# Performance work log

Measured on AMD Instinct MI355X. Metric: run time of the kernel, lower is better.

The kernel has to match this reference:

```python
import jax, jax.numpy as jnp
import numpy as np

TOP_K = 2
NORM_TOPK_PROB = True


def setup_inputs() -> dict:
    key = jax.random.key(0)
    k1, k2 = jax.random.split(key)
    hidden_states = jax.random.normal(k1, (4, 4096, 2048), dtype=jnp.float32)
    # gate weight [n_routed_experts, hidden_size], kaiming-uniform-like scale
    weight = jax.random.normal(k2, (64, 2048), dtype=jnp.float32) * 0.02
    return {"hidden_states": hidden_states, "weight": weight}


def reference(hidden_states, weight):
    bsz, seq_len, h = hidden_states.shape
    x = hidden_states.reshape(-1, h)                      # [T, H]
    logits = jnp.einsum("th,eh->te", x, weight)           # [T, E]
    scores = jax.nn.softmax(logits, axis=-1)              # [T, E]
    topk_weight, topk_idx = jax.lax.top_k(scores, TOP_K)  # [T, K] each
    if TOP_K > 1 and NORM_TOPK_PROB:
        topk_weight = topk_weight / (topk_weight.sum(axis=-1, keepdims=True) + 1e-20)
    return (topk_idx.reshape(bsz, seq_len, -1), topk_weight.reshape(bsz, seq_len, -1))
```

## Files before the change

kernel.cpp:

```cpp
#include <hip/hip_runtime.h>
#include <math.h>

#define H    2048
#define NE   64
#define TOKB 64
#define KC   32
#define NCH  64
#define NBUF 4
#define TAU  4.0e-3f
#define NEGF (-3.0e38f)

typedef __bf16 bf16x8 __attribute__((ext_vector_type(8)));
typedef float  f32x16 __attribute__((ext_vector_type(16)));

#define MFMA(a, b, c) __builtin_amdgcn_mfma_f32_32x32x16_bf16((a), (b), (c), 0, 0, 0)
#define LD4(p) (*reinterpret_cast<const float4*>(p))

__device__ __forceinline__ void cvt8(const float4 a, const float4 b,
                                     bf16x8& hi, bf16x8& lo) {
    const float v0 = a.x, v1 = a.y, v2 = a.z, v3 = a.w;
    const float v4 = b.x, v5 = b.y, v6 = b.z, v7 = b.w;
    hi[0] = (__bf16)v0; lo[0] = (__bf16)(v0 - (float)hi[0]);
    hi[1] = (__bf16)v1; lo[1] = (__bf16)(v1 - (float)hi[1]);
    hi[2] = (__bf16)v2; lo[2] = (__bf16)(v2 - (float)hi[2]);
    hi[3] = (__bf16)v3; lo[3] = (__bf16)(v3 - (float)hi[3]);
    hi[4] = (__bf16)v4; lo[4] = (__bf16)(v4 - (float)hi[4]);
    hi[5] = (__bf16)v5; lo[5] = (__bf16)(v5 - (float)hi[5]);
    hi[6] = (__bf16)v6; lo[6] = (__bf16)(v6 - (float)hi[6]);
    hi[7] = (__bf16)v7; lo[7] = (__bf16)(v7 - (float)hi[7]);
}

__device__ __forceinline__ void gll16(const void* g, void* l) {
    __builtin_amdgcn_global_load_lds(
        (const __attribute__((address_space(1))) void*)g,
        (__attribute__((address_space(3))) void*)l, 16, 0, 0);
}

__global__ __launch_bounds__(256) void prep_w(
    const float* __restrict__ w, __bf16* __restrict__ wp, int* __restrict__ wl)
{
    const int e   = blockIdx.x;
    const int tid = threadIdx.x;
    if (e == 0 && tid == 0) wl[0] = 0;
    const float4 a = LD4(&w[e * H + tid * 8]);
    const float4 b = LD4(&w[e * H + tid * 8 + 4]);
    bf16x8 hi, lo;
    cvt8(a, b, hi, lo);
    const int c  = tid >> 2;
    const int kk = (tid & 3) * 8;
    *reinterpret_cast<bf16x8*>(wp + e * 4096 + c * 64 + kk)      = hi;
    *reinterpret_cast<bf16x8*>(wp + e * 4096 + c * 64 + 32 + kk) = lo;
}

__global__ __launch_bounds__(256) void moe_gate_mfma(
    const float* __restrict__ x,
    const __bf16* __restrict__ wp,
    float* __restrict__ out, int woff,
    int* __restrict__ wl, int wlcap)
{
    __shared__ float4 lds4[NBUF][1024];

    const int tid  = threadIdx.x;
    const int lane = tid & 63;
    const int wv   = tid >> 6;
    const int mt   = wv >> 1;
    const int kh   = wv & 1;
    const int lo5  = lane & 31;
    const int hi5  = lane >> 5;
    const int t0   = blockIdx.x * TOKB;

    const char* sbase[4];
    #pragma unroll
    for (int s = 0; s < 4; ++s) {
        const int byte = (s * 256 + tid) * 16;
        if (byte < 8192) {
            const int row = byte >> 7;
            const int sl  = ((byte >> 4) & 7) ^ (row & 7);
            sbase[s] = (const char*)wp + (size_t)row * 8192 + sl * 16;
        } else {
            const int b   = byte - 8192;
            const int row = b >> 7;
            const int sl  = ((b >> 4) & 7) ^ (row & 7);
            sbase[s] = (const char*)x + (size_t)(t0 + row) * 8192 + sl * 16;
        }
    }

    f32x16 acc0, acc1;
    #pragma unroll
    for (int i = 0; i < 16; ++i) { acc0[i] = 0.f; acc1[i] = 0.f; }

    #pragma unroll
    for (int p = 0; p < 3; ++p)
        #pragma unroll
        for (int s = 0; s < 4; ++s)
            gll16(sbase[s] + p * 128, &lds4[p][s * 256 + wv * 64]);

    const int ra0 = lo5, ra1 = 32 + lo5;
    const int sA  = kh * 2 + hi5;
    const int offAh0 = ra0 * 128 + (((sA)     ^ (ra0 & 7)) << 4);
    const int offAl0 = ra0 * 128 + (((4 + sA) ^ (ra0 & 7)) << 4);
    const int offAh1 = ra1 * 128 + (((sA)     ^ (ra1 & 7)) << 4);
    const int offAl1 = ra1 * 128 + (((4 + sA) ^ (ra1 & 7)) << 4);
    const int rb  = mt * 32 + lo5;
    const int sB  = kh * 4 + hi5 * 2;
    const int offB0 = 8192 + rb * 128 + (((sB)     ^ (rb & 7)) << 4);
    const int offB1 = 8192 + rb * 128 + (((sB + 1) ^ (rb & 7)) << 4);

    for (int c = 0; c < NCH; ++c) {
        if (c < NCH - 2) {
            asm volatile("s_waitcnt vmcnt(8)" ::: "memory");
        } else if (c == NCH - 2) {
            asm volatile("s_waitcnt vmcnt(4)" ::: "memory");
        } else {
            asm volatile("s_waitcnt vmcnt(0)" ::: "memory");
        }
        __builtin_amdgcn_s_barrier();

        const char* bufb = (const char*)&lds4[c & 3][0];
        const bf16x8 ah0 = *reinterpret_cast<const bf16x8*>(bufb + offAh0);
        const bf16x8 al0 = *reinterpret_cast<const bf16x8*>(bufb + offAl0);
        const bf16x8 ah1 = *reinterpret_cast<const bf16x8*>(bufb + offAh1);
        const bf16x8 al1 = *reinterpret_cast<const bf16x8*>(bufb + offAl1);
        const float4 b1  = *reinterpret_cast<const float4*>(bufb + offB0);
        const float4 b2  = *reinterpret_cast<const float4*>(bufb + offB1);

        bf16x8 bh, bl;
        cvt8(b1, b2, bh, bl);

        acc0 = MFMA(ah0, bh, acc0);
        acc1 = MFMA(ah1, bh, acc1);
        acc0 = MFMA(ah0, bl, acc0);
        acc1 = MFMA(ah1, bl, acc1);
        acc0 = MFMA(al0, bh, acc0);
        acc1 = MFMA(al1, bh, acc1);

        if (c + 3 < NCH) {
            #pragma unroll
            for (int s = 0; s < 4; ++s)
                gll16(sbase[s] + (c + 3) * 128,
                      &lds4[(c + 3) & 3][s * 256 + wv * 64]);
        }
    }

    __syncthreads();
    float* S = reinterpret_cast<float*>(&lds4[0][0]);
    if (kh == 1) {
        const int base = (mt * 32 + lo5) * 65;
        #pragma unroll
        for (int r = 0; r < 16; ++r) {
            const int e0 = (r & 3) + 8 * (r >> 2) + 4 * hi5;
            S[base + e0]      = acc0[r];
            S[base + 32 + e0] = acc1[r];
        }
    }
    __syncthreads();
    if (kh == 1) return;
    {
        const int base = (mt * 32 + lo5) * 65;
        #pragma unroll
        for (int r = 0; r < 16; ++r) {
            const int e0 = (r & 3) + 8 * (r >> 2) + 4 * hi5;
            acc0[r] += S[base + e0];
            acc1[r] += S[base + 32 + e0];
        }
    }

    float m1 = NEGF, m2 = NEGF, m3 = NEGF;
    int   i1 = 0, i2 = 0;
    #pragma unroll
    for (int r = 0; r < 16; ++r) {
        const float v = acc0[r];
        const int   e = (r & 3) + 8 * (r >> 2) + 4 * hi5;
        if (v > m1)      { m3 = m2; m2 = m1; i2 = i1; m1 = v; i1 = e; }
        else if (v > m2) { m3 = m2; m2 = v; i2 = e; }
        else if (v > m3) { m3 = v; }
    }
    #pragma unroll
    for (int r = 0; r < 16; ++r) {
        const float v = acc1[r];
        const int   e = 32 + (r & 3) + 8 * (r >> 2) + 4 * hi5;
        if (v > m1)      { m3 = m2; m2 = m1; i2 = i1; m1 = v; i1 = e; }
        else if (v > m2) { m3 = m2; m2 = v; i2 = e; }
        else if (v > m3) { m3 = v; }
    }

    const float n1 = __shfl_xor(m1, 32), n2 = __shfl_xor(m2, 32), n3 = __shfl_xor(m3, 32);
    const int   j1 = __shfl_xor(i1, 32), j2 = __shfl_xor(i2, 32);

    float a1, a2, a3, b1, b2, b3; int ia1, ia2, ib1, ib2;
    const bool aF = (m1 > n1) || (m1 == n1 && i1 < j1);
    if (aF) { a1=m1; a2=m2; a3=m3; ia1=i1; ia2=i2; b1=n1; b2=n2; b3=n3; ib1=j1; ib2=j2; }
    else    { a1=n1; a2=n2; a3=n3; ia1=j1; ia2=j2; b1=m1; b2=m2; b3=m3; ib1=i1; ib2=i2; }

    const float o1 = a1; const int oi1 = ia1;
    float o2, o3; int oi2;
    const bool a2F = (a2 > b1) || (a2 == b1 && ia2 < ib1);
    if (a2F) { o2 = a2; oi2 = ia2; o3 = (a3 > b1) ? a3 : b1; }
    else     { o2 = b1; oi2 = ib1; o3 = (a2 > b2) ? a2 : b2; }

    if (hi5 == 0) {
        const int t = t0 + mt * 32 + lo5;
        const float r = expf(o2 - o1);
        const float s = 1.0f + r;
        out[2 * t + 0]        = (float)oi1;
        out[2 * t + 1]        = (float)oi2;
        out[woff + 2 * t + 0] = 1.0f / s;
        out[woff + 2 * t + 1] = r / s;
        if ((o1 - o2 < TAU) || (o2 - o3 < TAU)) {
            const int pos = atomicAdd(wl, 1);
            if (pos < wlcap) wl[1 + pos] = t;
        }
    }
}

__global__ __launch_bounds__(256) void moe_refine_fp64(
    const float* __restrict__ x, const float* __restrict__ w,
    float* __restrict__ out, int woff,
    const int* __restrict__ wl, int wlcap)
{
    __shared__ double Sd[3][NE];
    const int lane = threadIdx.x & 63;
    const int wv   = threadIdx.x >> 6;
    const int ks   = wv * 512;
    int cnt = wl[0];
    if (cnt > wlcap) cnt = wlcap;

    for (int i = blockIdx.x; i < cnt; i += gridDim.x) {
        const int t = wl[1 + i];

        const float4 xa = LD4(&x[(size_t)t * H + ks + lane * 4]);
        const float4 xb = LD4(&x[(size_t)t * H + ks + 256 + lane * 4]);
        const double x0 = xa.x, x1 = xa.y, x2 = xa.z, x3 = xa.w;
        const double x4 = xb.x, x5 = xb.y, x6 = xb.z, x7 = xb.w;

        double myacc = 0.0;
        #pragma unroll 4
        for (int e = 0; e < NE; ++e) {
            const float4 wa = LD4(&w[(size_t)e * H + ks + lane * 4]);
            const float4 wb = LD4(&w[(size_t)e * H + ks + 256 + lane * 4]);
            double sA = 0.0, sB = 0.0;
            sA = fma((double)wa.x, x0, sA); sA = fma((double)wa.y, x1, sA);
            sA = fma((double)wa.z, x2, sA); sA = fma((double)wa.w, x3, sA);
            sB = fma((double)wb.x, x4, sB); sB = fma((double)wb.y, x5, sB);
            sB = fma((double)wb.z, x6, sB); sB = fma((double)wb.w, x7, sB);
            double s = sA + sB;
            #pragma unroll
            for (int off = 1; off < 64; off <<= 1)
                s += __shfl_xor(s, off);
            if (lane == e) myacc = s;
        }

        if (wv > 0) Sd[wv - 1][lane] = myacc;
        __syncthreads();
        if (wv == 0) {
            const double acc = ((myacc + Sd[0][lane]) + Sd[1][lane]) + Sd[2][lane];

            double v = acc; int bi = lane;
            #pragma unroll
            for (int off = 32; off > 0; off >>= 1) {
                double ov = __shfl_xor(v, off);
                int    oi = __shfl_xor(bi, off);
                if (ov > v || (ov == v && oi < bi)) { v = ov; bi = oi; }
            }
            const double m1 = v; const int i1 = bi;

            double v2 = (lane == i1) ? -1.0e300 : acc; int b2 = lane;
            #pragma unroll
            for (int off = 32; off > 0; off >>= 1) {
                double ov = __shfl_xor(v2, off);
                int    oi = __shfl_xor(b2, off);
                if (ov > v2 || (ov == v2 && oi < b2)) { v2 = ov; b2 = oi; }
            }
            const double m2 = v2; const int i2 = b2;

            if (lane == 0) {
                const double r = exp(m2 - m1);
                const double s = 1.0 + r;
                out[2 * t + 0]        = (float)i1;
                out[2 * t + 1]        = (float)i2;
                out[woff + 2 * t + 0] = (float)(1.0 / s);
                out[woff + 2 * t + 1] = (float)(r / s);
            }
        }
        __syncthreads();
    }
}

extern "C" void kernel_launch(void* const* d_in, const int* in_sizes, int n_in,
                              void* d_out, int out_size, void* d_ws, size_t ws_size,
                              hipStream_t stream) {
    const float* x   = (const float*)d_in[0];
    const float* wgt = (const float*)d_in[1];
    float* out = (float*)d_out;

    const int T    = in_sizes[0] / H;
    const int woff = out_size / 2;

    int*    wl = (int*)d_ws;
    __bf16* wp = (__bf16*)((char*)d_ws + 131072);
    int wlcap = T;

    prep_w<<<dim3(NE), dim3(256), 0, stream>>>(wgt, wp, wl);

    moe_gate_mfma<<<dim3(T / TOKB), dim3(256), 0, stream>>>(
        x, wp, out, woff, wl, wlcap);

    moe_refine_fp64<<<dim3(512), dim3(256), 0, stream>>>(
        x, wgt, out, woff, wl, wlcap);
}
```

Before: 73.41 us.

## Double K-chunk width and split K across four waves per token tile

Each pipeline stage now covers 64 K elements instead of 32, and the block grows to 512 threads, with four waves splitting K per token half. Partial accumulators from three waves are reduced through LDS. The LDS ring grows to 128 KB of dynamic shared memory, and the next-chunk prefetch is issued before the MFMAs rather than after. The aim is more bytes in flight and fewer barriers per token tile, at the cost of one resident block per CU and a heavier cross-wave reduction.

```diff
diff --git a/kernel.cpp b/kernel.cpp
--- a/kernel.cpp
+++ b/kernel.cpp
@@ -4,8 +4,8 @@
 #define H    2048
 #define NE   64
 #define TOKB 64
-#define KC   32
-#define NCH  64
+#define KC   64
+#define NCH  32
 #define NBUF 4
 #define TAU  4.0e-3f
 #define NEGF (-3.0e38f)
@@ -52,19 +52,19 @@
     *reinterpret_cast<bf16x8*>(wp + e * 4096 + c * 64 + 32 + kk) = lo;
 }
 
-__global__ __launch_bounds__(256) void moe_gate_mfma(
+__global__ __launch_bounds__(512) void moe_gate_mfma(
     const float* __restrict__ x,
     const __bf16* __restrict__ wp,
     float* __restrict__ out, int woff,
     int* __restrict__ wl, int wlcap)
 {
-    __shared__ float4 lds4[NBUF][1024];
+    extern __shared__ char lds[];
 
     const int tid  = threadIdx.x;
     const int lane = tid & 63;
     const int wv   = tid >> 6;
-    const int mt   = wv >> 1;
-    const int kh   = wv & 1;
+    const int mt   = wv >> 2;
+    const int kq   = wv & 3;
     const int lo5  = lane & 31;
     const int hi5  = lane >> 5;
     const int t0   = blockIdx.x * TOKB;
@@ -72,15 +72,15 @@
     const char* sbase[4];
     #pragma unroll
     for (int s = 0; s < 4; ++s) {
-        const int byte = (s * 256 + tid) * 16;
-        if (byte < 8192) {
-            const int row = byte >> 7;
-            const int sl  = ((byte >> 4) & 7) ^ (row & 7);
+        const int byte = ((wv * 4 + s) * 64 + lane) * 16;
+        if (byte < 16384) {
+            const int row = byte >> 8;
+            const int sl  = ((byte >> 4) & 15) ^ (row & 15);
             sbase[s] = (const char*)wp + (size_t)row * 8192 + sl * 16;
         } else {
-            const int b   = byte - 8192;
-            const int row = b >> 7;
-            const int sl  = ((b >> 4) & 7) ^ (row & 7);
+            const int b   = byte - 16384;
+            const int row = b >> 8;
+            const int sl  = ((b >> 4) & 15) ^ (row & 15);
             sbase[s] = (const char*)x + (size_t)(t0 + row) * 8192 + sl * 16;
         }
     }
@@ -93,18 +93,18 @@
     for (int p = 0; p < 3; ++p)
         #pragma unroll
         for (int s = 0; s < 4; ++s)
-            gll16(sbase[s] + p * 128, &lds4[p][s * 256 + wv * 64]);
-
+            gll16(sbase[s] + p * 256, lds + p * 32768 + ((wv * 4 + s) * 64) * 16);
+
+    const int sa  = (kq >> 1) * 8 + (kq & 1) * 2 + hi5;
     const int ra0 = lo5, ra1 = 32 + lo5;
-    const int sA  = kh * 2 + hi5;
-    const int offAh0 = ra0 * 128 + (((sA)     ^ (ra0 & 7)) << 4);
-    const int offAl0 = ra0 * 128 + (((4 + sA) ^ (ra0 & 7)) << 4);
-    const int offAh1 = ra1 * 128 + (((sA)     ^ (ra1 & 7)) << 4);
-    const int offAl1 = ra1 * 128 + (((4 + sA) ^ (ra1 & 7)) << 4);
+    const int offAh0 = ra0 * 256 + (((sa)     ^ (ra0 & 15)) << 4);
+    const int offAl0 = ra0 * 256 + (((sa + 4) ^ (ra0 & 15)) << 4);
+    const int offAh1 = ra1 * 256 + (((sa)     ^ (ra1 & 15)) << 4);
+    const int offAl1 = ra1 * 256 + (((sa + 4) ^ (ra1 & 15)) << 4);
     const int rb  = mt * 32 + lo5;
-    const int sB  = kh * 4 + hi5 * 2;
-    const int offB0 = 8192 + rb * 128 + (((sB)     ^ (rb & 7)) << 4);
-    const int offB1 = 8192 + rb * 128 + (((sB + 1) ^ (rb & 7)) << 4);
+    const int sb  = kq * 4 + hi5 * 2;
+    const int offB0 = 16384 + rb * 256 + (((sb)     ^ (rb & 15)) << 4);
+    const int offB1 = 16384 + rb * 256 + (((sb + 1) ^ (rb & 15)) << 4);
 
     for (int c = 0; c < NCH; ++c) {
         if (c < NCH - 2) {
@@ -116,7 +116,7 @@
         }
         __builtin_amdgcn_s_barrier();
 
-        const char* bufb = (const char*)&lds4[c & 3][0];
+        const char* bufb = lds + (c & 3) * 32768;
         const bf16x8 ah0 = *reinterpret_cast<const bf16x8*>(bufb + offAh0);
         const bf16x8 al0 = *reinterpret_cast<const bf16x8*>(bufb + offAl0);
         const bf16x8 ah1 = *reinterpret_cast<const bf16x8*>(bufb + offAh1);
@@ -127,25 +127,25 @@
         bf16x8 bh, bl;
         cvt8(b1, b2, bh, bl);
 
+        if (c + 3 < NCH) {
+            #pragma unroll
+            for (int s = 0; s < 4; ++s)
+                gll16(sbase[s] + (c + 3) * 256,
+                      lds + ((c + 3) & 3) * 32768 + ((wv * 4 + s) * 64) * 16);
+        }
+
         acc0 = MFMA(ah0, bh, acc0);
         acc1 = MFMA(ah1, bh, acc1);
         acc0 = MFMA(ah0, bl, acc0);
         acc1 = MFMA(ah1, bl, acc1);
         acc0 = MFMA(al0, bh, acc0);
         acc1 = MFMA(al1, bh, acc1);
-
-        if (c + 3 < NCH) {
-            #pragma unroll
-            for (int s = 0; s < 4; ++s)
-                gll16(sbase[s] + (c + 3) * 128,
-                      &lds4[(c + 3) & 3][s * 256 + wv * 64]);
-        }
     }
 
     __syncthreads();
-    float* S = reinterpret_cast<float*>(&lds4[0][0]);
-    if (kh == 1) {
-        const int base = (mt * 32 + lo5) * 65;
+    float* S = reinterpret_cast<float*>(lds);
+    if (kq != 0) {
+        const int base = ((mt * 3 + (kq - 1)) * 32 + lo5) * 65;
         #pragma unroll
         for (int r = 0; r < 16; ++r) {
             const int e0 = (r & 3) + 8 * (r >> 2) + 4 * hi5;
@@ -154,9 +154,10 @@
         }
     }
     __syncthreads();
-    if (kh == 1) return;
-    {
-        const int base = (mt * 32 + lo5) * 65;
+    if (kq != 0) return;
+    #pragma unroll
+    for (int q = 0; q < 3; ++q) {
+        const int base = ((mt * 3 + q) * 32 + lo5) * 65;
         #pragma unroll
         for (int r = 0; r < 16; ++r) {
             const int e0 = (r & 3) + 8 * (r >> 2) + 4 * hi5;
@@ -300,9 +301,12 @@
     __bf16* wp = (__bf16*)((char*)d_ws + 131072);
     int wlcap = T;
 
+    (void)hipFuncSetAttribute((const void*)moe_gate_mfma,
+                              hipFuncAttributeMaxDynamicSharedMemorySize, 131072);
+
     prep_w<<<dim3(NE), dim3(256), 0, stream>>>(wgt, wp, wl);
 
-    moe_gate_mfma<<<dim3(T / TOKB), dim3(256), 0, stream>>>(
+    moe_gate_mfma<<<dim3(T / TOKB), dim3(512), 131072, stream>>>(
         x, wp, out, woff, wl, wlcap);
 
     moe_refine_fp64<<<dim3(512), dim3(256), 0, stream>>>(
```

Measured after the change: 60.78 us, median of 2. 17.2% less time.
